# Optimization experiments

Hardware: AMD Instinct MI355X
Metric: run time of the kernel (lower is better)

Reference implementation:

```python
import jax, jax.numpy as jnp
import numpy as np

TOP_K = 2
NUM_EXPERTS = 8


def setup_inputs() -> dict:
    key = jax.random.key(0)
    ks = jax.random.split(key, 9)
    B, S, N, H = 1, 8, 1024, 512
    E, I_moe, I_sh = NUM_EXPERTS, 2048 // TOP_K, 2048
    s = 0.02
    return {
        "hidden_states": jax.random.normal(ks[0], (B, S, N, H), dtype=jnp.float32),
        "gate_w": jax.random.normal(ks[1], (E, H), dtype=jnp.float32) * s,
        "expert_w1": jax.random.normal(ks[2], (E, I_moe, H), dtype=jnp.float32) * s,
        "expert_w2": jax.random.normal(ks[3], (E, H, I_moe), dtype=jnp.float32) * s,
        "expert_w3": jax.random.normal(ks[4], (E, I_moe, H), dtype=jnp.float32) * s,
        "shared_w1": jax.random.normal(ks[5], (I_sh, H), dtype=jnp.float32) * s,
        "shared_w2": jax.random.normal(ks[6], (H, I_sh), dtype=jnp.float32) * s,
        "shared_w3": jax.random.normal(ks[7], (I_sh, H), dtype=jnp.float32) * s,
        "shared_gate_w": jax.random.normal(ks[8], (1, H), dtype=jnp.float32) * s,
    }


def reference(hidden_states, gate_w, expert_w1, expert_w2, expert_w3,
              shared_w1, shared_w2, shared_w3, shared_gate_w):
    B, S, N, H = hidden_states.shape
    x = hidden_states.reshape(-1, H)                       # [T, H], T = B*S*N

    # Router: softmax in fp32, then top-k (norm_topk_prob=False).
    router_logits = x @ gate_w.T                           # [T, E]
    probs = jax.nn.softmax(router_logits.astype(jnp.float32), axis=-1)
    top_w, top_i = jax.lax.top_k(probs, TOP_K)             # [T, k]
    # Combine weight per (token, expert): zero for unselected experts.
    combine = jnp.sum(top_w[..., None] * jax.nn.one_hot(top_i, NUM_EXPERTS, dtype=probs.dtype), axis=1)
    combine = combine.astype(x.dtype)                      # [T, E]

    # Routed experts (SwiGLU FFN per expert), evaluated densely and masked
    # by the sparse combine weights (same math as gather/scatter dispatch).
    h1 = jnp.einsum('th,eih->tei', x, expert_w1)           # [T, E, I_moe]
    h3 = jnp.einsum('th,eih->tei', x, expert_w3)
    h = jax.nn.silu(h1) * h3
    expert_out = jnp.einsum('tei,ehi->teh', h, expert_w2)  # [T, E, H]
    moe_out = jnp.einsum('te,teh->th', combine, expert_out)

    # Shared expert with sigmoid gate.
    sh = (jax.nn.silu(x @ shared_w1.T) * (x @ shared_w3.T)) @ shared_w2.T
    sgate = jax.nn.sigmoid(x @ shared_gate_w.T)            # [T, 1]
    out = moe_out + sgate * sh

    return out.reshape(B, S, N, H), router_logits
```

## Files before the change

### kernel.cpp

```cpp
#include <hip/hip_runtime.h>
#include <hip/hip_bf16.h>
#include <stdint.h>
#include <math.h>

typedef __bf16 bf16;
typedef bf16 bf16x8 __attribute__((ext_vector_type(8)));
typedef bf16 bf16x4 __attribute__((ext_vector_type(4)));
typedef float f32x4 __attribute__((ext_vector_type(4)));
typedef unsigned int u32;

#define TOKENS 8192
#define HD 512
#define NE 8
#define IM 1024
#define ISH 2048
#define CAP 2560

__device__ __forceinline__ void gld16(const void* g, void* l) {
  __builtin_amdgcn_global_load_lds(
      (const __attribute__((address_space(1))) u32*)g,
      (__attribute__((address_space(3))) u32*)l, 16, 0, 0);
}

#define F4_E  (NE * IM * HD / 4)
#define F4_S  (ISH * HD / 4)
#define F4_C1 (F4_E)
#define F4_C2 (F4_C1 + F4_E)
#define F4_C3 (F4_C2 + F4_S)
#define F4_C4 (F4_C3 + F4_S)
#define F4_C5 (F4_C4 + F4_E)
#define F4_TOT (F4_C5 + F4_S)

__global__ void cvt_all(const float* __restrict__ e1, const float* __restrict__ e3,
                        const float* __restrict__ s1, const float* __restrict__ s3,
                        const float* __restrict__ e2, const float* __restrict__ s2,
                        bf16* __restrict__ dst) {
  int i = blockIdx.x * 256 + threadIdx.x;
  if (i >= F4_TOT) return;
  const float* s; int off;
  if (i < F4_C1)      { s = e1; off = i; }
  else if (i < F4_C2) { s = e3; off = i - F4_C1; }
  else if (i < F4_C3) { s = s1; off = i - F4_C2; }
  else if (i < F4_C4) { s = s3; off = i - F4_C3; }
  else if (i < F4_C5) { s = e2; off = i - F4_C4; }
  else                { s = s2; off = i - F4_C5; }
  const float4 v = ((const float4*)s)[off];
  bf16x4 o;
  o.x = (bf16)v.x; o.y = (bf16)v.y; o.z = (bf16)v.z; o.w = (bf16)v.w;
  ((bf16x4*)dst)[i] = o;
}

__launch_bounds__(256)
__global__ void router_k(const float* __restrict__ x, const float* __restrict__ gw,
                         const float* __restrict__ sgw, float* __restrict__ logits,
                         float* __restrict__ sgate, int* __restrict__ topi,
                         float* __restrict__ topw, int* __restrict__ counts,
                         bf16* __restrict__ xb) {
  if (blockIdx.x == 0 && threadIdx.x < NE) counts[threadIdx.x] = 0;
  __shared__ float gws[9][512];
  for (int i = threadIdx.x; i < 9 * 512; i += 256) {
    int r = i >> 9, c = i & 511;
    float v = (r < 8) ? gw[i] : sgw[c];
    gws[r][((c & 7) << 6) | (c >> 3)] = v;
  }
  __syncthreads();
  int wave = threadIdx.x >> 6, lane = threadIdx.x & 63;
  int t = blockIdx.x * 4 + wave;
  const float* xp = x + (size_t)t * HD + lane * 8;
  float4 va = *(const float4*)xp;
  float4 vb = *(const float4*)(xp + 4);
  float xv[8] = {va.x, va.y, va.z, va.w, vb.x, vb.y, vb.z, vb.w};
  {
    bf16x8 xo;
#pragma unroll
    for (int j = 0; j < 8; j++) xo[j] = (bf16)xv[j];
    *(bf16x8*)(xb + (size_t)t * HD + lane * 8) = xo;
  }
  float acc[9];
#pragma unroll
  for (int e = 0; e < 9; e++) {
    float a = 0.f;
#pragma unroll
    for (int j = 0; j < 8; j++) a = fmaf(xv[j], gws[e][j * 64 + lane], a);
    acc[e] = a;
  }
#pragma unroll
  for (int off = 32; off > 0; off >>= 1) {
#pragma unroll
    for (int e = 0; e < 9; e++) acc[e] += __shfl_down(acc[e], off);
  }
  if (lane == 0) {
    float mx = acc[0];
#pragma unroll
    for (int e = 1; e < 8; e++) mx = fmaxf(mx, acc[e]);
    float p[8], sum = 0.f;
#pragma unroll
    for (int e = 0; e < 8; e++) { p[e] = expf(acc[e] - mx); sum += p[e]; }
    float inv = 1.f / sum;
    int i0 = 0; float b0 = p[0];
#pragma unroll
    for (int e = 1; e < 8; e++) if (p[e] > b0) { b0 = p[e]; i0 = e; }
    int i1 = -1; float b1 = -1.f;
#pragma unroll
    for (int e = 0; e < 8; e++) if (e != i0 && p[e] > b1) { b1 = p[e]; i1 = e; }
#pragma unroll
    for (int e = 0; e < 8; e++) logits[(size_t)t * 8 + e] = acc[e];
    topi[2 * t] = i0; topi[2 * t + 1] = i1;
    topw[2 * t] = b0 * inv; topw[2 * t + 1] = b1 * inv;
    sgate[t] = 1.f / (1.f + expf(-acc[8]));
  }
}

__launch_bounds__(256)
__global__ void dispatch_k(const int* __restrict__ topi, const float* __restrict__ topw,
                           int* __restrict__ counts, int* __restrict__ tok,
                           float* __restrict__ wl, int* __restrict__ pos) {
  __shared__ int lcnt[NE];
  __shared__ int lbase[NE];
  int tid = threadIdx.x;
  if (tid < NE) lcnt[tid] = 0;
  __syncthreads();
  int t = blockIdx.x * 256 + tid;
  int e0 = topi[2 * t], e1 = topi[2 * t + 1];
  float w0 = topw[2 * t], w1 = topw[2 * t + 1];
  int r0 = atomicAdd(&lcnt[e0], 1);
  int r1 = atomicAdd(&lcnt[e1], 1);
  __syncthreads();
  if (tid < NE) lbase[tid] = atomicAdd(&counts[tid], lcnt[tid]);
  __syncthreads();
  int p0 = lbase[e0] + r0;
  int p1 = lbase[e1] + r1;
  if (p0 < CAP) { tok[e0 * CAP + p0] = t; wl[e0 * CAP + p0] = w0; }
  if (p1 < CAP) { tok[e1 * CAP + p1] = t; wl[e1 * CAP + p1] = w1; }
  pos[2 * t]     = (p0 < CAP) ? e0 * CAP + p0 : -1;
  pos[2 * t + 1] = (p1 < CAP) ? e1 * CAP + p1 : -1;
}

__launch_bounds__(256, 4)
__global__ void gemm1_k(const bf16* __restrict__ X, const int* __restrict__ tokl,
                        const int* __restrict__ counts,
                        const bf16* __restrict__ e1w, const bf16* __restrict__ e3w,
                        const bf16* __restrict__ s1w, const bf16* __restrict__ s3w,
                        bf16* __restrict__ hmoe, bf16* __restrict__ hsh) {
  const bf16 *W1, *W3;
  bf16* Hout;
  const int* tl = nullptr;
  int cnt = 0, m0, n0, N;
  bool gather;
  int y = blockIdx.y;
  if (y < 160) {
    int e = y / 20, mt = y % 20;
    cnt = min(counts[e], CAP);
    if (mt * 128 >= cnt) return;
    gather = true;
    tl = tokl + e * CAP;
    W1 = e1w + (size_t)e * IM * HD;
    W3 = e3w + (size_t)e * IM * HD;
    Hout = hmoe + (size_t)e * CAP * IM;
    N = IM; m0 = mt * 128; n0 = blockIdx.x * 64;
  } else {
    int s = y - 160;
    gather = false;
    W1 = s1w; W3 = s3w; Hout = hsh; N = ISH;
    m0 = (s >> 1) * 128;
    n0 = ((s & 1) * 16 + blockIdx.x) * 64;
  }

  __shared__ __align__(16) bf16 As[2][128 * 32];
  __shared__ __align__(16) bf16 B1s[2][64 * 32];
  __shared__ __align__(16) bf16 B3s[2][64 * 32];

  int tid = threadIdx.x;
  int sr = tid >> 2;
  int colb = (tid & 3) * 16;
  int ar0, ar1;
  if (gather) {
    ar0 = tl[min(m0 + sr, cnt - 1)];
    ar1 = tl[min(m0 + 64 + sr, cnt - 1)];
  } else { ar0 = m0 + sr; ar1 = m0 + 64 + sr; }
  const char* apa = (const char*)(X + (size_t)ar0 * HD) + colb;
  const char* apb = (const char*)(X + (size_t)ar1 * HD) + colb;
  const char* bp1 = (const char*)(W1 + (size_t)(n0 + sr) * HD) + colb;
  const char* bp3 = (const char*)(W3 + (size_t)(n0 + sr) * HD) + colb;
  char* lA0a = (char*)&As[0][0] + tid * 16;
  char* lA0b = (char*)&As[1][0] + tid * 16;
  char* lA1a = (char*)&As[0][0] + 4096 + tid * 16;
  char* lA1b = (char*)&As[1][0] + 4096 + tid * 16;
  char* lB1a = (char*)&B1s[0][0] + tid * 16;
  char* lB1b = (char*)&B1s[1][0] + tid * 16;
  char* lB3a = (char*)&B3s[0][0] + tid * 16;
  char* lB3b = (char*)&B3s[1][0] + tid * 16;

  int wid = tid >> 6, lane = tid & 63;
  int wm = (wid >> 1) * 64, wn = (wid & 1) * 32;
  int lrow = lane & 15, lq = lane >> 4;

  f32x4 acc1[4][2] = {};
  f32x4 acc3[4][2] = {};

  for (int kb = 0; kb < 1024; kb += 128) {
    __syncthreads();
    gld16(apa + kb, lA0a);      gld16(apa + kb + 64, lA0b);
    gld16(apb + kb, lA1a);      gld16(apb + kb + 64, lA1b);
    gld16(bp1 + kb, lB1a);      gld16(bp1 + kb + 64, lB1b);
    gld16(bp3 + kb, lB3a);      gld16(bp3 + kb + 64, lB3b);
    __syncthreads();
#pragma unroll
    for (int ks = 0; ks < 2; ks++) {
      bf16x8 a[4], b1[2], b3[2];
#pragma unroll
      for (int i = 0; i < 4; i++)
        a[i] = *(const bf16x8*)&As[ks][(wm + i * 16 + lrow) * 32 + lq * 8];
#pragma unroll
      for (int j = 0; j < 2; j++) {
        b1[j] = *(const bf16x8*)&B1s[ks][(wn + j * 16 + lrow) * 32 + lq * 8];
        b3[j] = *(const bf16x8*)&B3s[ks][(wn + j * 16 + lrow) * 32 + lq * 8];
      }
#pragma unroll
      for (int i = 0; i < 4; i++)
#pragma unroll
        for (int j = 0; j < 2; j++) {
          acc1[i][j] = __builtin_amdgcn_mfma_f32_16x16x32_bf16(a[i], b1[j], acc1[i][j], 0, 0, 0);
          acc3[i][j] = __builtin_amdgcn_mfma_f32_16x16x32_bf16(a[i], b3[j], acc3[i][j], 0, 0, 0);
        }
    }
  }

#pragma unroll
  for (int i = 0; i < 4; i++)
#pragma unroll
    for (int r = 0; r < 4; r++) {
      int row = m0 + wm + i * 16 + lq * 4 + r;
#pragma unroll
      for (int j = 0; j < 2; j++) {
        float v1 = acc1[i][j][r], v3 = acc3[i][j][r];
        float hv = v1 / (1.f + __expf(-v1)) * v3;
        Hout[(size_t)row * N + (n0 + wn + j * 16 + lrow)] = (bf16)hv;
      }
    }
}

__launch_bounds__(256, 4)
__global__ void gemm2_k(const bf16* __restrict__ hmoe, const bf16* __restrict__ hsh,
                        const bf16* __restrict__ e2w, const bf16* __restrict__ s2w,
                        const float* __restrict__ wll, const int* __restrict__ counts,
                        bf16* __restrict__ yslot, bf16* __restrict__ ysh) {
  const bf16 *Hin, *W2;
  const float* wlp = nullptr;
  bf16* Yout;
  int cnt = 0, m0, K;
  bool weighted;
  int y = blockIdx.y;
  if (y < 64) {
    weighted = false;
    Hin = hsh; W2 = s2w; Yout = ysh; K = ISH; m0 = y * 128;
  } else {
    int e = (y - 64) / 20, mt = (y - 64) % 20;
    cnt = min(counts[e], CAP);
    if (mt * 128 >= cnt) return;
    weighted = true;
    Hin = hmoe + (size_t)e * CAP * IM;
    W2 = e2w + (size_t)e * HD * IM;
    wlp = wll + e * CAP;
    Yout = yslot + (size_t)e * CAP * HD;
    K = IM; m0 = mt * 128;
  }
  int n0 = blockIdx.x * 128;

  __shared__ __align__(16) bf16 As[128 * 32];
  __shared__ __align__(16) bf16 Bs[128 * 32];

  int tid = threadIdx.x;
  int sr = tid >> 2;
  int colb = (tid & 3) * 16;
  const char* apa = (const char*)(Hin + (size_t)(m0 + sr) * K) + colb;
  const char* apb = (const char*)(Hin + (size_t)(m0 + 64 + sr) * K) + colb;
  const char* bpa = (const char*)(W2 + (size_t)(n0 + sr) * K) + colb;
  const char* bpb = (const char*)(W2 + (size_t)(n0 + 64 + sr) * K) + colb;
  char* lA0 = (char*)As + tid * 16;
  char* lA1 = (char*)As + 4096 + tid * 16;
  char* lB0 = (char*)Bs + tid * 16;
  char* lB1 = (char*)Bs + 4096 + tid * 16;

  int wid = tid >> 6, lane = tid & 63;
  int wm = (wid >> 1) * 64, wn = (wid & 1) * 64;
  int lrow = lane & 15, lq = lane >> 4;

  f32x4 acc[4][4] = {};

  for (int kb = 0; kb < K * 2; kb += 64) {
    __syncthreads();
    gld16(apa + kb, lA0);
    gld16(apb + kb, lA1);
    gld16(bpa + kb, lB0);
    gld16(bpb + kb, lB1);
    __syncthreads();
    bf16x8 a[4], b[4];
#pragma unroll
    for (int i = 0; i < 4; i++) {
      a[i] = *(const bf16x8*)&As[(wm + i * 16 + lrow) * 32 + lq * 8];
      b[i] = *(const bf16x8*)&Bs[(wn + i * 16 + lrow) * 32 + lq * 8];
    }
#pragma unroll
    for (int i = 0; i < 4; i++)
#pragma unroll
      for (int j = 0; j < 4; j++)
        acc[i][j] = __builtin_amdgcn_mfma_f32_16x16x32_bf16(a[i], b[j], acc[i][j], 0, 0, 0);
  }

#pragma unroll
  for (int i = 0; i < 4; i++)
#pragma unroll
    for (int r = 0; r < 4; r++) {
      int row = m0 + wm + i * 16 + lq * 4 + r;
      float w = weighted ? ((row < cnt) ? wlp[row] : 0.f) : 1.f;
      bf16* op = Yout + (size_t)row * HD;
#pragma unroll
      for (int j = 0; j < 4; j++)
        op[n0 + wn + j * 16 + lrow] = (bf16)(w * acc[i][j][r]);
    }
}

__launch_bounds__(256)
__global__ void combine_k(const bf16* __restrict__ yslot, const bf16* __restrict__ ysh,
                          const int* __restrict__ pos, const float* __restrict__ sgate,
                          float* __restrict__ out) {
  int wave = threadIdx.x >> 6, lane = threadIdx.x & 63;
  int t = blockIdx.x * 4 + wave;
  int p0 = pos[2 * t], p1 = pos[2 * t + 1];
  float g = sgate[t];
  int col = lane * 8;
  float acc[8];
  {
    const bf16x8 s = *(const bf16x8*)(ysh + (size_t)t * HD + col);
#pragma unroll
    for (int i = 0; i < 8; i++) acc[i] = g * (float)s[i];
  }
  if (p0 >= 0) {
    const bf16x8 v = *(const bf16x8*)(yslot + (size_t)p0 * HD + col);
#pragma unroll
    for (int i = 0; i < 8; i++) acc[i] += (float)v[i];
  }
  if (p1 >= 0) {
    const bf16x8 v = *(const bf16x8*)(yslot + (size_t)p1 * HD + col);
#pragma unroll
    for (int i = 0; i < 8; i++) acc[i] += (float)v[i];
  }
  float* op = out + (size_t)t * HD + col;
#pragma unroll
  for (int i = 0; i < 8; i++) op[i] = acc[i];
}

extern "C" void kernel_launch(void* const* d_in, const int* in_sizes, int n_in,
                              void* d_out, int out_size, void* d_ws, size_t ws_size,
                              hipStream_t stream) {
  const float* x   = (const float*)d_in[0];
  const float* gw  = (const float*)d_in[1];
  const float* ew1 = (const float*)d_in[2];
  const float* ew2 = (const float*)d_in[3];
  const float* ew3 = (const float*)d_in[4];
  const float* sw1 = (const float*)d_in[5];
  const float* sw2 = (const float*)d_in[6];
  const float* sw3 = (const float*)d_in[7];
  const float* sgw = (const float*)d_in[8];
  float* out = (float*)d_out;
  float* logits = out + (size_t)TOKENS * HD;

  char* w = (char*)d_ws;
  bf16* xb  = (bf16*)w; w += (size_t)TOKENS * HD * 2;
  bf16* e1b = (bf16*)w; w += (size_t)NE * IM * HD * 2;
  bf16* e3b = (bf16*)w; w += (size_t)NE * IM * HD * 2;
  bf16* s1b = (bf16*)w; w += (size_t)ISH * HD * 2;
  bf16* s3b = (bf16*)w; w += (size_t)ISH * HD * 2;
  bf16* e2b = (bf16*)w; w += (size_t)NE * HD * IM * 2;
  bf16* s2b = (bf16*)w; w += (size_t)HD * ISH * 2;
  float* sgate = (float*)w; w += TOKENS * 4;
  int*   topi  = (int*)w;   w += TOKENS * 2 * 4;
  float* topw  = (float*)w; w += TOKENS * 2 * 4;
  int*   counts = (int*)w;  w += 256;
  int*   tok   = (int*)w;   w += NE * CAP * 4;
  float* wl    = (float*)w; w += NE * CAP * 4;
  int*   pos   = (int*)w;   w += TOKENS * 2 * 4;
  bf16* hmoe = (bf16*)w; w += (size_t)NE * CAP * IM * 2;
  bf16* hsh  = (bf16*)w; w += (size_t)TOKENS * ISH * 2;
  bf16* yslot = xb;
  bf16* ysh   = (bf16*)((char*)xb + (size_t)NE * CAP * HD * 2);

  hipLaunchKernelGGL(cvt_all, dim3((F4_TOT + 255) / 256), dim3(256), 0, stream,
                     ew1, ew3, sw1, sw3, ew2, sw2, e1b);
  hipLaunchKernelGGL(router_k, dim3(TOKENS / 4), dim3(256), 0, stream,
                     x, gw, sgw, logits, sgate, topi, topw, counts, xb);
  hipLaunchKernelGGL(dispatch_k, dim3(TOKENS / 256), dim3(256), 0, stream,
                     topi, topw, counts, tok, wl, pos);
  hipLaunchKernelGGL(gemm1_k, dim3(16, 160 + 128), dim3(256), 0, stream,
                     xb, tok, counts, e1b, e3b, s1b, s3b, hmoe, hsh);
  hipLaunchKernelGGL(gemm2_k, dim3(4, 64 + 160), dim3(256), 0, stream,
                     hmoe, hsh, e2b, s2b, wl, counts, yslot, ysh);
  hipLaunchKernelGGL(combine_k, dim3(TOKENS / 4), dim3(256), 0, stream,
                     yslot, ysh, pos, sgate, out);
}
```

Baseline: 286.3 us.

## Use 32x32x16 MFMA in GEMMs and fuse weight conversion into router kernel

Both expert GEMM kernels move from 16x16x32 to 32x32x16 bf16 MFMA tiles. This reduces LDS fragment loads per MFMA and changes the accumulator layout and epilogue indexing to match. The separate fp32-to-bf16 weight conversion kernel is merged into the router kernel as extra blocks, each converting four strided elements. This removes one launch and lets the router run concurrently with the conversion. It also adds register pressure from the larger accumulators and makes the merged kernel's blocks uneven in work.

New measurement: 298.7 us. 4.3% more time.

```diff
diff --git a/kernel.cpp b/kernel.cpp
--- a/kernel.cpp
+++ b/kernel.cpp
@@ -7,6 +7,7 @@
 typedef bf16 bf16x8 __attribute__((ext_vector_type(8)));
 typedef bf16 bf16x4 __attribute__((ext_vector_type(4)));
 typedef float f32x4 __attribute__((ext_vector_type(4)));
+typedef float f32x16 __attribute__((ext_vector_type(16)));
 typedef unsigned int u32;
 
 #define TOKENS 8192
@@ -22,6 +23,9 @@
       (__attribute__((address_space(3))) u32*)l, 16, 0, 0);
 }
 
+#define RT_BLOCKS (TOKENS / 4)
+#define CVT_BLOCKS 3840
+#define CVT_STRIDE (CVT_BLOCKS * 256)
 #define F4_E  (NE * IM * HD / 4)
 #define F4_S  (ISH * HD / 4)
 #define F4_C1 (F4_E)
@@ -31,31 +35,34 @@
 #define F4_C5 (F4_C4 + F4_E)
 #define F4_TOT (F4_C5 + F4_S)
 
-__global__ void cvt_all(const float* __restrict__ e1, const float* __restrict__ e3,
-                        const float* __restrict__ s1, const float* __restrict__ s3,
-                        const float* __restrict__ e2, const float* __restrict__ s2,
-                        bf16* __restrict__ dst) {
-  int i = blockIdx.x * 256 + threadIdx.x;
-  if (i >= F4_TOT) return;
-  const float* s; int off;
-  if (i < F4_C1)      { s = e1; off = i; }
-  else if (i < F4_C2) { s = e3; off = i - F4_C1; }
-  else if (i < F4_C3) { s = s1; off = i - F4_C2; }
-  else if (i < F4_C4) { s = s3; off = i - F4_C3; }
-  else if (i < F4_C5) { s = e2; off = i - F4_C4; }
-  else                { s = s2; off = i - F4_C5; }
-  const float4 v = ((const float4*)s)[off];
-  bf16x4 o;
-  o.x = (bf16)v.x; o.y = (bf16)v.y; o.z = (bf16)v.z; o.w = (bf16)v.w;
-  ((bf16x4*)dst)[i] = o;
-}
-
 __launch_bounds__(256)
-__global__ void router_k(const float* __restrict__ x, const float* __restrict__ gw,
-                         const float* __restrict__ sgw, float* __restrict__ logits,
-                         float* __restrict__ sgate, int* __restrict__ topi,
-                         float* __restrict__ topw, int* __restrict__ counts,
-                         bf16* __restrict__ xb) {
+__global__ void router_cvt_k(const float* __restrict__ x, const float* __restrict__ gw,
+                             const float* __restrict__ sgw, float* __restrict__ logits,
+                             float* __restrict__ sgate, int* __restrict__ topi,
+                             float* __restrict__ topw, int* __restrict__ counts,
+                             bf16* __restrict__ xb,
+                             const float* __restrict__ e1, const float* __restrict__ e3,
+                             const float* __restrict__ s1, const float* __restrict__ s3,
+                             const float* __restrict__ e2, const float* __restrict__ s2,
+                             bf16* __restrict__ wdst) {
+  if (blockIdx.x >= RT_BLOCKS) {
+    int idx = (blockIdx.x - RT_BLOCKS) * 256 + threadIdx.x;
+#pragma unroll
+    for (int it = 0; it < 4; it++, idx += CVT_STRIDE) {
+      const float* s; int off;
+      if (idx < F4_C1)      { s = e1; off = idx; }
+      else if (idx < F4_C2) { s = e3; off = idx - F4_C1; }
+      else if (idx < F4_C3) { s = s1; off = idx - F4_C2; }
+      else if (idx < F4_C4) { s = s3; off = idx - F4_C3; }
+      else if (idx < F4_C5) { s = e2; off = idx - F4_C4; }
+      else                  { s = s2; off = idx - F4_C5; }
+      const float4 v = ((const float4*)s)[off];
+      bf16x4 o;
+      o.x = (bf16)v.x; o.y = (bf16)v.y; o.z = (bf16)v.z; o.w = (bf16)v.w;
+      ((bf16x4*)wdst)[idx] = o;
+    }
+    return;
+  }
   if (blockIdx.x == 0 && threadIdx.x < NE) counts[threadIdx.x] = 0;
   __shared__ float gws[9][512];
   for (int i = threadIdx.x; i < 9 * 512; i += 256) {
@@ -193,10 +200,10 @@
 
   int wid = tid >> 6, lane = tid & 63;
   int wm = (wid >> 1) * 64, wn = (wid & 1) * 32;
-  int lrow = lane & 15, lq = lane >> 4;
-
-  f32x4 acc1[4][2] = {};
-  f32x4 acc3[4][2] = {};
+  int lr = lane & 31, lq = lane >> 5;
+
+  f32x16 acc1[2] = {};
+  f32x16 acc3[2] = {};
 
   for (int kb = 0; kb < 1024; kb += 128) {
     __syncthreads();
@@ -207,36 +214,29 @@
     __syncthreads();
 #pragma unroll
     for (int ks = 0; ks < 2; ks++) {
-      bf16x8 a[4], b1[2], b3[2];
-#pragma unroll
-      for (int i = 0; i < 4; i++)
-        a[i] = *(const bf16x8*)&As[ks][(wm + i * 16 + lrow) * 32 + lq * 8];
-#pragma unroll
-      for (int j = 0; j < 2; j++) {
-        b1[j] = *(const bf16x8*)&B1s[ks][(wn + j * 16 + lrow) * 32 + lq * 8];
-        b3[j] = *(const bf16x8*)&B3s[ks][(wn + j * 16 + lrow) * 32 + lq * 8];
+#pragma unroll
+      for (int s = 0; s < 2; s++) {
+        int co = s * 16 + lq * 8;
+        bf16x8 a0 = *(const bf16x8*)&As[ks][(wm + lr) * 32 + co];
+        bf16x8 a1 = *(const bf16x8*)&As[ks][(wm + 32 + lr) * 32 + co];
+        bf16x8 b1 = *(const bf16x8*)&B1s[ks][(wn + lr) * 32 + co];
+        bf16x8 b3 = *(const bf16x8*)&B3s[ks][(wn + lr) * 32 + co];
+        acc1[0] = __builtin_amdgcn_mfma_f32_32x32x16_bf16(a0, b1, acc1[0], 0, 0, 0);
+        acc1[1] = __builtin_amdgcn_mfma_f32_32x32x16_bf16(a1, b1, acc1[1], 0, 0, 0);
+        acc3[0] = __builtin_amdgcn_mfma_f32_32x32x16_bf16(a0, b3, acc3[0], 0, 0, 0);
+        acc3[1] = __builtin_amdgcn_mfma_f32_32x32x16_bf16(a1, b3, acc3[1], 0, 0, 0);
       }
-#pragma unroll
-      for (int i = 0; i < 4; i++)
-#pragma unroll
-        for (int j = 0; j < 2; j++) {
-          acc1[i][j] = __builtin_amdgcn_mfma_f32_16x16x32_bf16(a[i], b1[j], acc1[i][j], 0, 0, 0);
-          acc3[i][j] = __builtin_amdgcn_mfma_f32_16x16x32_bf16(a[i], b3[j], acc3[i][j], 0, 0, 0);
-        }
     }
   }
 
 #pragma unroll
-  for (int i = 0; i < 4; i++)
-#pragma unroll
-    for (int r = 0; r < 4; r++) {
-      int row = m0 + wm + i * 16 + lq * 4 + r;
-#pragma unroll
-      for (int j = 0; j < 2; j++) {
-        float v1 = acc1[i][j][r], v3 = acc3[i][j][r];
-        float hv = v1 / (1.f + __expf(-v1)) * v3;
-        Hout[(size_t)row * N + (n0 + wn + j * 16 + lrow)] = (bf16)hv;
-      }
+  for (int i = 0; i < 2; i++)
+#pragma unroll
+    for (int r = 0; r < 16; r++) {
+      int row = m0 + wm + i * 32 + 4 * lq + (r & 3) + 8 * (r >> 2);
+      float v1 = acc1[i][r], v3 = acc3[i][r];
+      float hv = v1 / (1.f + __expf(-v1)) * v3;
+      Hout[(size_t)row * N + (n0 + wn + lr)] = (bf16)hv;
     }
 }
 
@@ -284,9 +284,9 @@
 
   int wid = tid >> 6, lane = tid & 63;
   int wm = (wid >> 1) * 64, wn = (wid & 1) * 64;
-  int lrow = lane & 15, lq = lane >> 4;
-
-  f32x4 acc[4][4] = {};
+  int lr = lane & 31, lq = lane >> 5;
+
+  f32x16 acc[2][2] = {};
 
   for (int kb = 0; kb < K * 2; kb += 64) {
     __syncthreads();
@@ -295,29 +295,29 @@
     gld16(bpa + kb, lB0);
     gld16(bpb + kb, lB1);
     __syncthreads();
-    bf16x8 a[4], b[4];
-#pragma unroll
-    for (int i = 0; i < 4; i++) {
-      a[i] = *(const bf16x8*)&As[(wm + i * 16 + lrow) * 32 + lq * 8];
-      b[i] = *(const bf16x8*)&Bs[(wn + i * 16 + lrow) * 32 + lq * 8];
+#pragma unroll
+    for (int s = 0; s < 2; s++) {
+      int co = s * 16 + lq * 8;
+      bf16x8 a0 = *(const bf16x8*)&As[(wm + lr) * 32 + co];
+      bf16x8 a1 = *(const bf16x8*)&As[(wm + 32 + lr) * 32 + co];
+      bf16x8 b0 = *(const bf16x8*)&Bs[(wn + lr) * 32 + co];
+      bf16x8 b1 = *(const bf16x8*)&Bs[(wn + 32 + lr) * 32 + co];
+      acc[0][0] = __builtin_amdgcn_mfma_f32_32x32x16_bf16(a0, b0, acc[0][0], 0, 0, 0);
+      acc[0][1] = __builtin_amdgcn_mfma_f32_32x32x16_bf16(a0, b1, acc[0][1], 0, 0, 0);
+      acc[1][0] = __builtin_amdgcn_mfma_f32_32x32x16_bf16(a1, b0, acc[1][0], 0, 0, 0);
+      acc[1][1] = __builtin_amdgcn_mfma_f32_32x32x16_bf16(a1, b1, acc[1][1], 0, 0, 0);
     }
-#pragma unroll
-    for (int i = 0; i < 4; i++)
-#pragma unroll
-      for (int j = 0; j < 4; j++)
-        acc[i][j] = __builtin_amdgcn_mfma_f32_16x16x32_bf16(a[i], b[j], acc[i][j], 0, 0, 0);
-  }
-
-#pragma unroll
-  for (int i = 0; i < 4; i++)
-#pragma unroll
-    for (int r = 0; r < 4; r++) {
-      int row = m0 + wm + i * 16 + lq * 4 + r;
+  }
+
+#pragma unroll
+  for (int i = 0; i < 2; i++)
+#pragma unroll
+    for (int r = 0; r < 16; r++) {
+      int row = m0 + wm + i * 32 + 4 * lq + (r & 3) + 8 * (r >> 2);
       float w = weighted ? ((row < cnt) ? wlp[row] : 0.f) : 1.f;
-      bf16* op = Yout + (size_t)row * HD;
-#pragma unroll
-      for (int j = 0; j < 4; j++)
-        op[n0 + wn + j * 16 + lrow] = (bf16)(w * acc[i][j][r]);
+      bf16* op = Yout + (size_t)row * HD + n0 + wn + lr;
+      op[0]  = (bf16)(w * acc[i][0][r]);
+      op[32] = (bf16)(w * acc[i][1][r]);
     }
 }
 
@@ -386,10 +386,9 @@
   bf16* yslot = xb;
   bf16* ysh   = (bf16*)((char*)xb + (size_t)NE * CAP * HD * 2);
 
-  hipLaunchKernelGGL(cvt_all, dim3((F4_TOT + 255) / 256), dim3(256), 0, stream,
+  hipLaunchKernelGGL(router_cvt_k, dim3(RT_BLOCKS + CVT_BLOCKS), dim3(256), 0, stream,
+                     x, gw, sgw, logits, sgate, topi, topw, counts, xb,
                      ew1, ew3, sw1, sw3, ew2, sw2, e1b);
-  hipLaunchKernelGGL(router_k, dim3(TOKENS / 4), dim3(256), 0, stream,
-                     x, gw, sgw, logits, sgate, topi, topw, counts, xb);
   hipLaunchKernelGGL(dispatch_k, dim3(TOKENS / 256), dim3(256), 0, stream,
                      topi, topw, counts, tok, wl, pos);
   hipLaunchKernelGGL(gemm1_k, dim3(16, 160 + 128), dim3(256), 0, stream,
```

## Fuse weight conversion into router kernel and widen gemm1 N-tile to 128

Applied to the files above, without the earlier changes.

Merges the fp32-to-bf16 weight conversion into the router launch as extra blocks, each converting four strided chunks, so the two can overlap and one launch is removed. gemm1 widens its N tile from 64 to 128 per block with 4x4 MFMA accumulators per wave, doubling B-tile LDS and register use and lowering launch bounds occupancy from 4 to 2. The wider tile reuses each A tile across more output columns, at the cost of fewer blocks and more register pressure. Expert blocks with blockIdx.x beyond 8 exit early.

New measurement: 315.2 us. +10.1%, slower.

```diff
diff --git a/kernel.cpp b/kernel.cpp
--- a/kernel.cpp
+++ b/kernel.cpp
@@ -22,6 +22,9 @@
       (__attribute__((address_space(3))) u32*)l, 16, 0, 0);
 }
 
+#define RT_BLOCKS (TOKENS / 4)
+#define CVT_BLOCKS 3840
+#define CVT_STRIDE (CVT_BLOCKS * 256)
 #define F4_E  (NE * IM * HD / 4)
 #define F4_S  (ISH * HD / 4)
 #define F4_C1 (F4_E)
@@ -31,31 +34,34 @@
 #define F4_C5 (F4_C4 + F4_E)
 #define F4_TOT (F4_C5 + F4_S)
 
-__global__ void cvt_all(const float* __restrict__ e1, const float* __restrict__ e3,
-                        const float* __restrict__ s1, const float* __restrict__ s3,
-                        const float* __restrict__ e2, const float* __restrict__ s2,
-                        bf16* __restrict__ dst) {
-  int i = blockIdx.x * 256 + threadIdx.x;
-  if (i >= F4_TOT) return;
-  const float* s; int off;
-  if (i < F4_C1)      { s = e1; off = i; }
-  else if (i < F4_C2) { s = e3; off = i - F4_C1; }
-  else if (i < F4_C3) { s = s1; off = i - F4_C2; }
-  else if (i < F4_C4) { s = s3; off = i - F4_C3; }
-  else if (i < F4_C5) { s = e2; off = i - F4_C4; }
-  else                { s = s2; off = i - F4_C5; }
-  const float4 v = ((const float4*)s)[off];
-  bf16x4 o;
-  o.x = (bf16)v.x; o.y = (bf16)v.y; o.z = (bf16)v.z; o.w = (bf16)v.w;
-  ((bf16x4*)dst)[i] = o;
-}
-
 __launch_bounds__(256)
-__global__ void router_k(const float* __restrict__ x, const float* __restrict__ gw,
-                         const float* __restrict__ sgw, float* __restrict__ logits,
-                         float* __restrict__ sgate, int* __restrict__ topi,
-                         float* __restrict__ topw, int* __restrict__ counts,
-                         bf16* __restrict__ xb) {
+__global__ void router_cvt_k(const float* __restrict__ x, const float* __restrict__ gw,
+                             const float* __restrict__ sgw, float* __restrict__ logits,
+                             float* __restrict__ sgate, int* __restrict__ topi,
+                             float* __restrict__ topw, int* __restrict__ counts,
+                             bf16* __restrict__ xb,
+                             const float* __restrict__ e1, const float* __restrict__ e3,
+                             const float* __restrict__ s1, const float* __restrict__ s3,
+                             const float* __restrict__ e2, const float* __restrict__ s2,
+                             bf16* __restrict__ wdst) {
+  if (blockIdx.x >= RT_BLOCKS) {
+    int idx = (blockIdx.x - RT_BLOCKS) * 256 + threadIdx.x;
+#pragma unroll
+    for (int it = 0; it < 4; it++, idx += CVT_STRIDE) {
+      const float* s; int off;
+      if (idx < F4_C1)      { s = e1; off = idx; }
+      else if (idx < F4_C2) { s = e3; off = idx - F4_C1; }
+      else if (idx < F4_C3) { s = s1; off = idx - F4_C2; }
+      else if (idx < F4_C4) { s = s3; off = idx - F4_C3; }
+      else if (idx < F4_C5) { s = e2; off = idx - F4_C4; }
+      else                  { s = s2; off = idx - F4_C5; }
+      const float4 v = ((const float4*)s)[off];
+      bf16x4 o;
+      o.x = (bf16)v.x; o.y = (bf16)v.y; o.z = (bf16)v.z; o.w = (bf16)v.w;
+      ((bf16x4*)wdst)[idx] = o;
+    }
+    return;
+  }
   if (blockIdx.x == 0 && threadIdx.x < NE) counts[threadIdx.x] = 0;
   __shared__ float gws[9][512];
   for (int i = threadIdx.x; i < 9 * 512; i += 256) {
@@ -136,7 +142,7 @@
   pos[2 * t + 1] = (p1 < CAP) ? e1 * CAP + p1 : -1;
 }
 
-__launch_bounds__(256, 4)
+__launch_bounds__(256, 2)
 __global__ void gemm1_k(const bf16* __restrict__ X, const int* __restrict__ tokl,
                         const int* __restrict__ counts,
                         const bf16* __restrict__ e1w, const bf16* __restrict__ e3w,
@@ -149,6 +155,7 @@
   bool gather;
   int y = blockIdx.y;
   if (y < 160) {
+    if (blockIdx.x >= IM / 128) return;
     int e = y / 20, mt = y % 20;
     cnt = min(counts[e], CAP);
     if (mt * 128 >= cnt) return;
@@ -157,18 +164,17 @@
     W1 = e1w + (size_t)e * IM * HD;
     W3 = e3w + (size_t)e * IM * HD;
     Hout = hmoe + (size_t)e * CAP * IM;
-    N = IM; m0 = mt * 128; n0 = blockIdx.x * 64;
+    N = IM; m0 = mt * 128; n0 = blockIdx.x * 128;
   } else {
     int s = y - 160;
     gather = false;
     W1 = s1w; W3 = s3w; Hout = hsh; N = ISH;
-    m0 = (s >> 1) * 128;
-    n0 = ((s & 1) * 16 + blockIdx.x) * 64;
+    m0 = s * 128; n0 = blockIdx.x * 128;
   }
 
   __shared__ __align__(16) bf16 As[2][128 * 32];
-  __shared__ __align__(16) bf16 B1s[2][64 * 32];
-  __shared__ __align__(16) bf16 B3s[2][64 * 32];
+  __shared__ __align__(16) bf16 B1s[2][128 * 32];
+  __shared__ __align__(16) bf16 B3s[2][128 * 32];
 
   int tid = threadIdx.x;
   int sr = tid >> 2;
@@ -180,46 +186,54 @@
   } else { ar0 = m0 + sr; ar1 = m0 + 64 + sr; }
   const char* apa = (const char*)(X + (size_t)ar0 * HD) + colb;
   const char* apb = (const char*)(X + (size_t)ar1 * HD) + colb;
-  const char* bp1 = (const char*)(W1 + (size_t)(n0 + sr) * HD) + colb;
-  const char* bp3 = (const char*)(W3 + (size_t)(n0 + sr) * HD) + colb;
+  const char* bp1a = (const char*)(W1 + (size_t)(n0 + sr) * HD) + colb;
+  const char* bp1b = (const char*)(W1 + (size_t)(n0 + 64 + sr) * HD) + colb;
+  const char* bp3a = (const char*)(W3 + (size_t)(n0 + sr) * HD) + colb;
+  const char* bp3b = (const char*)(W3 + (size_t)(n0 + 64 + sr) * HD) + colb;
   char* lA0a = (char*)&As[0][0] + tid * 16;
   char* lA0b = (char*)&As[1][0] + tid * 16;
   char* lA1a = (char*)&As[0][0] + 4096 + tid * 16;
   char* lA1b = (char*)&As[1][0] + 4096 + tid * 16;
-  char* lB1a = (char*)&B1s[0][0] + tid * 16;
-  char* lB1b = (char*)&B1s[1][0] + tid * 16;
-  char* lB3a = (char*)&B3s[0][0] + tid * 16;
-  char* lB3b = (char*)&B3s[1][0] + tid * 16;
+  char* lB1a0 = (char*)&B1s[0][0] + tid * 16;
+  char* lB1a1 = (char*)&B1s[0][0] + 4096 + tid * 16;
+  char* lB1b0 = (char*)&B1s[1][0] + tid * 16;
+  char* lB1b1 = (char*)&B1s[1][0] + 4096 + tid * 16;
+  char* lB3a0 = (char*)&B3s[0][0] + tid * 16;
+  char* lB3a1 = (char*)&B3s[0][0] + 4096 + tid * 16;
+  char* lB3b0 = (char*)&B3s[1][0] + tid * 16;
+  char* lB3b1 = (char*)&B3s[1][0] + 4096 + tid * 16;
 
   int wid = tid >> 6, lane = tid & 63;
-  int wm = (wid >> 1) * 64, wn = (wid & 1) * 32;
+  int wm = (wid >> 1) * 64, wn = (wid & 1) * 64;
   int lrow = lane & 15, lq = lane >> 4;
 
-  f32x4 acc1[4][2] = {};
-  f32x4 acc3[4][2] = {};
+  f32x4 acc1[4][4] = {};
+  f32x4 acc3[4][4] = {};
 
   for (int kb = 0; kb < 1024; kb += 128) {
     __syncthreads();
-    gld16(apa + kb, lA0a);      gld16(apa + kb + 64, lA0b);
-    gld16(apb + kb, lA1a);      gld16(apb + kb + 64, lA1b);
-    gld16(bp1 + kb, lB1a);      gld16(bp1 + kb + 64, lB1b);
-    gld16(bp3 + kb, lB3a);      gld16(bp3 + kb + 64, lB3b);
+    gld16(apa + kb, lA0a);       gld16(apa + kb + 64, lA0b);
+    gld16(apb + kb, lA1a);       gld16(apb + kb + 64, lA1b);
+    gld16(bp1a + kb, lB1a0);     gld16(bp1a + kb + 64, lB1b0);
+    gld16(bp1b + kb, lB1a1);     gld16(bp1b + kb + 64, lB1b1);
+    gld16(bp3a + kb, lB3a0);     gld16(bp3a + kb + 64, lB3b0);
+    gld16(bp3b + kb, lB3a1);     gld16(bp3b + kb + 64, lB3b1);
     __syncthreads();
 #pragma unroll
     for (int ks = 0; ks < 2; ks++) {
-      bf16x8 a[4], b1[2], b3[2];
+      bf16x8 a[4], b1[4], b3[4];
 #pragma unroll
       for (int i = 0; i < 4; i++)
         a[i] = *(const bf16x8*)&As[ks][(wm + i * 16 + lrow) * 32 + lq * 8];
 #pragma unroll
-      for (int j = 0; j < 2; j++) {
+      for (int j = 0; j < 4; j++) {
         b1[j] = *(const bf16x8*)&B1s[ks][(wn + j * 16 + lrow) * 32 + lq * 8];
         b3[j] = *(const bf16x8*)&B3s[ks][(wn + j * 16 + lrow) * 32 + lq * 8];
       }
 #pragma unroll
       for (int i = 0; i < 4; i++)
 #pragma unroll
-        for (int j = 0; j < 2; j++) {
+        for (int j = 0; j < 4; j++) {
           acc1[i][j] = __builtin_amdgcn_mfma_f32_16x16x32_bf16(a[i], b1[j], acc1[i][j], 0, 0, 0);
           acc3[i][j] = __builtin_amdgcn_mfma_f32_16x16x32_bf16(a[i], b3[j], acc3[i][j], 0, 0, 0);
         }
@@ -232,7 +246,7 @@
     for (int r = 0; r < 4; r++) {
       int row = m0 + wm + i * 16 + lq * 4 + r;
 #pragma unroll
-      for (int j = 0; j < 2; j++) {
+      for (int j = 0; j < 4; j++) {
         float v1 = acc1[i][j][r], v3 = acc3[i][j][r];
         float hv = v1 / (1.f + __expf(-v1)) * v3;
         Hout[(size_t)row * N + (n0 + wn + j * 16 + lrow)] = (bf16)hv;
@@ -386,13 +400,12 @@
   bf16* yslot = xb;
   bf16* ysh   = (bf16*)((char*)xb + (size_t)NE * CAP * HD * 2);
 
-  hipLaunchKernelGGL(cvt_all, dim3((F4_TOT + 255) / 256), dim3(256), 0, stream,
+  hipLaunchKernelGGL(router_cvt_k, dim3(RT_BLOCKS + CVT_BLOCKS), dim3(256), 0, stream,
+                     x, gw, sgw, logits, sgate, topi, topw, counts, xb,
                      ew1, ew3, sw1, sw3, ew2, sw2, e1b);
-  hipLaunchKernelGGL(router_k, dim3(TOKENS / 4), dim3(256), 0, stream,
-                     x, gw, sgw, logits, sgate, topi, topw, counts, xb);
   hipLaunchKernelGGL(dispatch_k, dim3(TOKENS / 256), dim3(256), 0, stream,
                      topi, topw, counts, tok, wl, pos);
-  hipLaunchKernelGGL(gemm1_k, dim3(16, 160 + 128), dim3(256), 0, stream,
+  hipLaunchKernelGGL(gemm1_k, dim3(16, 160 + 64), dim3(256), 0, stream,
                      xb, tok, counts, e1b, e3b, s1b, s3b, hmoe, hsh);
   hipLaunchKernelGGL(gemm2_k, dim3(4, 64 + 160), dim3(256), 0, stream,
                      hmoe, hsh, e2b, s2b, wl, counts, yslot, ysh);
```
